# Performance work log

Measured on AMD Instinct MI355X. Metric: run time of the kernel, lower is better.

Reference implementation:

```python
import jax, jax.numpy as jnp
import numpy as np

B, T, D, H = 8, 1024, 1024, 16
HD = D // H
SCALE = HD ** -0.5


def setup_inputs() -> dict:
    key = jax.random.key(0)
    ks = jax.random.split(key, 5)
    s = 0.02
    return {
        "hidden_states": jax.random.normal(ks[0], (B, T, D), jnp.float32),
        "Wq": jax.random.normal(ks[1], (D, D), jnp.float32) * s,
        "bq": jnp.zeros((D,), jnp.float32),
        "Wk": jax.random.normal(ks[2], (D, D), jnp.float32) * s,
        "bk": jnp.zeros((D,), jnp.float32),
        "Wv": jax.random.normal(ks[3], (D, D), jnp.float32) * s,
        "bv": jnp.zeros((D,), jnp.float32),
        "Wo": jax.random.normal(ks[4], (D, D), jnp.float32) * s,
        "bo": jnp.zeros((D,), jnp.float32),
    }


def _split_heads(x):
    # [B, T, D] -> [B, H, T, HD]
    return x.reshape(B, T, H, HD).transpose(0, 2, 1, 3)


def reference(hidden_states, Wq, bq, Wk, bk, Wv, bv, Wo, bo):
    q = _split_heads((hidden_states @ Wq + bq) * SCALE)
    k = _split_heads(hidden_states @ Wk + bk)
    v = _split_heads(hidden_states @ Wv + bv)
    # [B, H, T, T] attention scores
    scores = jnp.einsum("bhqd,bhkd->bhqk", q, k)
    probs = jax.nn.softmax(scores, axis=-1)
    attn = jnp.einsum("bhqk,bhkd->bhqd", probs, v)
    attn = attn.transpose(0, 2, 1, 3).reshape(B, T, D)
    return attn @ Wo + bo
```

## Files before the change

kernel.cpp:

```cpp
#include <hip/hip_runtime.h>

typedef unsigned short u16;
typedef __attribute__((ext_vector_type(4))) float f32x4;
typedef __attribute__((ext_vector_type(8))) __bf16 bf16x8;
typedef __attribute__((ext_vector_type(4))) __bf16 bf16x4;
typedef __attribute__((ext_vector_type(4))) unsigned short u16x4;
typedef __attribute__((ext_vector_type(8))) unsigned short u16x8;

static __device__ __forceinline__ u16 f2bf(float f) {
    union { float f; unsigned u; } v; v.f = f;
    unsigned r = v.u + 0x7FFFu + ((v.u >> 16) & 1u);
    return (u16)(r >> 16);
}

static __device__ __forceinline__ float exp2f_fast(float x) {
    float r; asm("v_exp_f32 %0, %1" : "=v"(r) : "v"(x)); return r;
}

static __device__ __forceinline__ void gload16(const u16* g, u16* l) {
    __builtin_amdgcn_global_load_lds(
        (const __attribute__((address_space(1))) unsigned int*)g,
        (__attribute__((address_space(3))) unsigned int*)l, 16, 0, 0);
}

template<int N> static __device__ __forceinline__ void vm_wait() {
    if constexpr (N >= 8)      asm volatile("s_waitcnt vmcnt(8)" ::: "memory");
    else if constexpr (N == 6) asm volatile("s_waitcnt vmcnt(6)" ::: "memory");
    else if constexpr (N == 4) asm volatile("s_waitcnt vmcnt(4)" ::: "memory");
    else if constexpr (N == 3) asm volatile("s_waitcnt vmcnt(3)" ::: "memory");
    else if constexpr (N == 2) asm volatile("s_waitcnt vmcnt(2)" ::: "memory");
    else                       asm volatile("s_waitcnt vmcnt(0)" ::: "memory");
}

#define SWZ64(row, ec) (((row) * 64) + ((((ec) ^ ((row) & 7))) << 3))

__global__ __launch_bounds__(256) void k_prep(
    const float* __restrict__ hs, u16* __restrict__ Xb,
    const float* __restrict__ W0, const float* __restrict__ W1,
    const float* __restrict__ W2, const float* __restrict__ W3,
    u16* __restrict__ T0, u16* __restrict__ T1, u16* __restrict__ T2, u16* __restrict__ T3,
    float s0) {
    __shared__ float tile[32][33];
    const int id = blockIdx.x;
    const int tid = threadIdx.x;
    if (id < 8192) {
        size_t i = (size_t)id * 256 + tid;
        float4 v = ((const float4*)hs)[i];
        u16x4 o; o[0] = f2bf(v.x); o[1] = f2bf(v.y); o[2] = f2bf(v.z); o[3] = f2bf(v.w);
        *(u16x4*)(Xb + i * 4) = o;
        return;
    }
    const int wid = id - 8192;
    const int z = wid >> 10, rem = wid & 1023;
    const int n0 = (rem & 31) * 32, k0 = (rem >> 5) * 32;
    const float* W; u16* Tt; float sc;
    switch (z) {
        case 0:  W = W0; Tt = T0; sc = s0;  break;
        case 1:  W = W1; Tt = T1; sc = 1.f; break;
        case 2:  W = W2; Tt = T2; sc = 1.f; break;
        default: W = W3; Tt = T3; sc = 1.f; break;
    }
    int r = tid >> 3, c = (tid & 7) * 4;
    float4 v = *(const float4*)(W + (size_t)(k0 + r) * 1024 + n0 + c);
    tile[r][c] = v.x; tile[r][c + 1] = v.y; tile[r][c + 2] = v.z; tile[r][c + 3] = v.w;
    __syncthreads();
    u16x4 o;
    o[0] = f2bf(tile[c][r] * sc);
    o[1] = f2bf(tile[c + 1][r] * sc);
    o[2] = f2bf(tile[c + 2][r] * sc);
    o[3] = f2bf(tile[c + 3][r] * sc);
    *(u16x4*)(Tt + (size_t)(n0 + r) * 1024 + k0 + c) = o;
}

template<int BN>
__global__ __launch_bounds__(512, 2) void k_g256(
    const u16* __restrict__ A, const u16* __restrict__ Bt,
    const float* __restrict__ bias, const float* __restrict__ biasK, float qscale,
    u16* __restrict__ obf, u16* __restrict__ obK, float* __restrict__ of32,
    int ldc, int bias_row, int nblk, int mode) {
    constexpr int WN = (BN == 256) ? 4 : 2;
    constexpr int WAVE_M = (BN == 256) ? 128 : 64;
    constexpr int M_REP = WAVE_M / 16;
    constexpr int BCALLS = BN / 128;
    constexpr int LPT = 2 + BCALLS;
    constexpr int ASLOT = 256 * 32;
    constexpr int BSLOT = BN * 32;
    __shared__ u16 As[4 * ASLOT];
    __shared__ u16 Bs[4 * BSLOT];
    const int tid = threadIdx.x;
    const int l = tid & 63, w = tid >> 6;
    const int mw = w / WN, nw = w % WN;
    const int fr = l & 15, gg = l >> 4, f4 = gg * 4;
    const int id = blockIdx.x;
    const int swz = (id & 7) * 32 + (id >> 3);
    const int bm = swz / nblk, bn = swz % nblk;
    const size_t m0 = (size_t)bm * 256, n0v = (size_t)bn * BN;

    const int srow = w * 16 + (l >> 2);
    const int schk = ((l & 3) ^ ((l >> 3) & 3)) * 8;
    const u16* agp0 = A + (m0 + srow) * 1024 + schk;
    const u16* agp1 = A + (m0 + 128 + srow) * 1024 + schk;
    const u16* bgp0 = Bt + (n0v + srow) * 1024 + schk;
    const u16* bgp1 = (BN == 256) ? Bt + (n0v + 128 + srow) * 1024 + schk : bgp0;
    const int ldst = w * 512 + l * 8;

    const int fchk = (gg ^ ((fr >> 1) & 3)) * 8;
    int aoff[8], boff[4];
#pragma unroll
    for (int mt = 0; mt < 8; ++mt) aoff[mt] = (mw * WAVE_M + mt * 16 + fr) * 32 + fchk;
#pragma unroll
    for (int nt = 0; nt < 4; ++nt) boff[nt] = (nw * 64 + nt * 16 + fr) * 32 + fchk;

    f32x4 acc[8][4] = {};

#define PSTG(S, J)                                                              \
    gload16(agp0 + (size_t)(J) * 32, As + (S) * ASLOT + ldst);                  \
    gload16(agp1 + (size_t)(J) * 32, As + (S) * ASLOT + 4096 + ldst);           \
    gload16(bgp0 + (size_t)(J) * 32, Bs + (S) * BSLOT + ldst);                  \
    if constexpr (BN == 256)                                                    \
        gload16(bgp1 + (size_t)(J) * 32, Bs + (S) * BSLOT + 4096 + ldst);
    PSTG(0, 0) PSTG(1, 1) PSTG(2, 2)
#undef PSTG

#define TILE(S, J, VMN, STG)                                                    \
    {                                                                           \
        vm_wait<VMN>();                                                         \
        __builtin_amdgcn_s_barrier();                                           \
        bf16x8 afr[4], bfr[4];                                                  \
        _Pragma("unroll")                                                       \
        for (int nt = 0; nt < 4; ++nt)                                          \
            bfr[nt] = *(const bf16x8*)(&Bs[(S) * BSLOT + boff[nt]]);            \
        _Pragma("unroll")                                                       \
        for (int mt = 0; mt < 4; ++mt)                                          \
            afr[mt] = *(const bf16x8*)(&As[(S) * ASLOT + aoff[mt]]);            \
        if constexpr (STG) {                                                    \
            gload16(agp0 + (size_t)((J) + 3) * 32, As + (((S) + 3) & 3) * ASLOT + ldst);        \
            gload16(agp1 + (size_t)((J) + 3) * 32, As + (((S) + 3) & 3) * ASLOT + 4096 + ldst); \
            if constexpr (BN == 128)                                            \
                gload16(bgp0 + (size_t)((J) + 3) * 32, Bs + (((S) + 3) & 3) * BSLOT + ldst);    \
        }                                                                       \
        __builtin_amdgcn_s_barrier();                                           \
        asm volatile("s_waitcnt lgkmcnt(0)" ::: "memory");                      \
        __builtin_amdgcn_sched_barrier(0);                                      \
        __builtin_amdgcn_s_setprio(1);                                          \
        _Pragma("unroll")                                                       \
        for (int mt = 0; mt < 4; ++mt)                                          \
            _Pragma("unroll")                                                   \
            for (int nt = 0; nt < 4; ++nt)                                      \
                acc[mt][nt] = __builtin_amdgcn_mfma_f32_16x16x32_bf16(afr[mt], bfr[nt], acc[mt][nt], 0, 0, 0); \
        __builtin_amdgcn_s_setprio(0);                                          \
        if constexpr (BN == 256) {                                              \
            _Pragma("unroll")                                                   \
            for (int mt = 0; mt < 4; ++mt)                                      \
                afr[mt] = *(const bf16x8*)(&As[(S) * ASLOT + aoff[4 + mt]]);    \
            if constexpr (STG) {                                                \
                gload16(bgp0 + (size_t)((J) + 3) * 32, Bs + (((S) + 3) & 3) * BSLOT + ldst);        \
                gload16(bgp1 + (size_t)((J) + 3) * 32, Bs + (((S) + 3) & 3) * BSLOT + 4096 + ldst); \
            }                                                                   \
            __builtin_amdgcn_s_barrier();                                       \
            asm volatile("s_waitcnt lgkmcnt(0)" ::: "memory");                  \
            __builtin_amdgcn_sched_barrier(0);                                  \
            __builtin_amdgcn_s_setprio(1);                                      \
            _Pragma("unroll")                                                   \
            for (int mt = 0; mt < 4; ++mt)                                      \
                _Pragma("unroll")                                               \
                for (int nt = 0; nt < 4; ++nt)                                  \
                    acc[4 + mt][nt] = __builtin_amdgcn_mfma_f32_16x16x32_bf16(afr[mt], bfr[nt], acc[4 + mt][nt], 0, 0, 0); \
            __builtin_amdgcn_s_setprio(0);                                      \
        }                                                                       \
    }

#pragma unroll 1
    for (int jb = 0; jb < 28; jb += 4) {
        TILE(0, jb + 0, (2 * LPT), true)
        TILE(1, jb + 1, (2 * LPT), true)
        TILE(2, jb + 2, (2 * LPT), true)
        TILE(3, jb + 3, (2 * LPT), true)
    }
    TILE(0, 28, (2 * LPT), true)
    TILE(1, 29, (2 * LPT), false)
    TILE(2, 30, LPT, false)
    TILE(3, 31, 0, false)
#undef TILE

    const int mrow0 = (int)m0 + mw * WAVE_M;
    const int ncol0 = (int)n0v + nw * 64;
    if (mode == 1) {
#pragma unroll
        for (int mt = 0; mt < M_REP; ++mt)
#pragma unroll
            for (int nt = 0; nt < 4; ++nt) {
                const int col = ncol0 + nt * 16 + fr;
                const int seg = col >> 10, colm = col & 1023;
                const float bb = (seg ? biasK[colm] : bias[colm] * qscale);
                u16* op = seg ? obK : obf;
#pragma unroll
                for (int r = 0; r < 4; ++r)
                    op[(size_t)(mrow0 + mt * 16 + f4 + r) * 1024 + colm] = f2bf(acc[mt][nt][r] + bb);
            }
    } else if (mode == 2) {
#pragma unroll
        for (int mt = 0; mt < M_REP; ++mt) {
            float rb_[4];
#pragma unroll
            for (int r = 0; r < 4; ++r) rb_[r] = bias[mrow0 + mt * 16 + f4 + r];
#pragma unroll
            for (int nt = 0; nt < 4; ++nt) {
                const int col = ncol0 + nt * 16 + fr;
                const int colp = (col & ~31) | (((col >> 2) & 3) << 3) |
                                 (((col >> 4) & 1) << 2) | (col & 3);
#pragma unroll
                for (int r = 0; r < 4; ++r) {
                    const size_t row = (size_t)(mrow0 + mt * 16 + f4 + r);
                    obf[row * (size_t)ldc + colp] = f2bf(acc[mt][nt][r] + rb_[r]);
                }
            }
        }
    } else {
#pragma unroll
        for (int mt = 0; mt < M_REP; ++mt) {
            float rb_[4];
#pragma unroll
            for (int r = 0; r < 4; ++r)
                rb_[r] = bias_row ? bias[mrow0 + mt * 16 + f4 + r] : 0.f;
#pragma unroll
            for (int nt = 0; nt < 4; ++nt) {
                const int col = ncol0 + nt * 16 + fr;
                const float cb = bias_row ? 0.f : bias[col];
#pragma unroll
                for (int r = 0; r < 4; ++r) {
                    const size_t row = (size_t)(mrow0 + mt * 16 + f4 + r);
                    const float vv = acc[mt][nt][r] + cb + rb_[r];
                    if (of32) of32[row * (size_t)ldc + col] = vv;
                    else      obf[row * (size_t)ldc + col] = f2bf(vv);
                }
            }
        }
    }
}

static __device__ __forceinline__ void qk_tile(const u16* Ks, int fr, int gg,
                                               bf16x8 qA0, bf16x8 qA1, bf16x8 qB0, bf16x8 qB1,
                                               float mA, float mB, f32x4 sA[4], f32x4 sB[4]) {
    __builtin_amdgcn_s_setprio(1);
#pragma unroll
    for (int nt = 0; nt < 4; ++nt) {
        const int rk = nt * 16 + fr;
        const bf16x8 kf0 = *(const bf16x8*)(&Ks[SWZ64(rk, gg)]);
        const bf16x8 kf1 = *(const bf16x8*)(&Ks[SWZ64(rk, gg + 4)]);
        f32x4 z = {-mA, -mA, -mA, -mA};
        z = __builtin_amdgcn_mfma_f32_16x16x32_bf16(kf0, qA0, z, 0, 0, 0);
        z = __builtin_amdgcn_mfma_f32_16x16x32_bf16(kf1, qA1, z, 0, 0, 0);
        sA[nt] = z;
        f32x4 y = {-mB, -mB, -mB, -mB};
        y = __builtin_amdgcn_mfma_f32_16x16x32_bf16(kf0, qB0, y, 0, 0, 0);
        y = __builtin_amdgcn_mfma_f32_16x16x32_bf16(kf1, qB1, y, 0, 0, 0);
        sB[nt] = y;
    }
    __builtin_amdgcn_s_setprio(0);
}

static __device__ __forceinline__ void sm_tile(const f32x4 s[4], f32x4 o[4],
                                               float& m, float& lsum, bf16x4 p[4]) {
    float mymax = s[0][0];
#pragma unroll
    for (int nt = 0; nt < 4; ++nt)
#pragma unroll
        for (int r = 0; r < 4; ++r) mymax = fmaxf(mymax, s[nt][r]);
    float ps = 0.f;
#pragma unroll
    for (int nt = 0; nt < 4; ++nt)
#pragma unroll
        for (int r = 0; r < 4; ++r) {
            const float pp = exp2f_fast(s[nt][r]);
            ps += pp; p[nt][r] = (__bf16)pp;
        }
    if (__builtin_expect(__any(mymax > 11.0f), 0)) {
        float rm = fmaxf(mymax, __shfl_xor(mymax, 16, 64));
        rm = fmaxf(rm, __shfl_xor(rm, 32, 64));
        const float d = fmaxf(rm, 0.f);
        const float fac = exp2f_fast(-d);
        m += d; lsum *= fac;
#pragma unroll
        for (int mt = 0; mt < 4; ++mt)
#pragma unroll
            for (int r = 0; r < 4; ++r) o[mt][r] *= fac;
        ps = 0.f;
#pragma unroll
        for (int nt = 0; nt < 4; ++nt)
#pragma unroll
            for (int r = 0; r < 4; ++r) {
                const float pp = exp2f_fast(s[nt][r] - d);
                ps += pp; p[nt][r] = (__bf16)pp;
            }
    }
    lsum += ps;
}

static __device__ __forceinline__ void pv_tile(const u16* Vs, int fr, int gg,
                                               const bf16x4 pA[4], const bf16x4 pB[4],
                                               f32x4 oA[4], f32x4 oB[4]) {
    const bf16x8 BA0 = __builtin_shufflevector(pA[0], pA[1], 0, 1, 2, 3, 4, 5, 6, 7);
    const bf16x8 BA1 = __builtin_shufflevector(pA[2], pA[3], 0, 1, 2, 3, 4, 5, 6, 7);
    const bf16x8 BB0 = __builtin_shufflevector(pB[0], pB[1], 0, 1, 2, 3, 4, 5, 6, 7);
    const bf16x8 BB1 = __builtin_shufflevector(pB[2], pB[3], 0, 1, 2, 3, 4, 5, 6, 7);
    __builtin_amdgcn_s_setprio(1);
#pragma unroll
    for (int mt = 0; mt < 4; ++mt) {
        const int rv = mt * 16 + fr;
        const bf16x8 vk0 = *(const bf16x8*)(&Vs[SWZ64(rv, gg)]);
        const bf16x8 vk1 = *(const bf16x8*)(&Vs[SWZ64(rv, gg + 4)]);
        oA[mt] = __builtin_amdgcn_mfma_f32_16x16x32_bf16(vk0, BA0, oA[mt], 0, 0, 0);
        oA[mt] = __builtin_amdgcn_mfma_f32_16x16x32_bf16(vk1, BA1, oA[mt], 0, 0, 0);
        oB[mt] = __builtin_amdgcn_mfma_f32_16x16x32_bf16(vk0, BB0, oB[mt], 0, 0, 0);
        oB[mt] = __builtin_amdgcn_mfma_f32_16x16x32_bf16(vk1, BB1, oB[mt], 0, 0, 0);
    }
    __builtin_amdgcn_s_setprio(0);
}

__global__ __launch_bounds__(256, 2) void k_flash(const u16* __restrict__ Q, const u16* __restrict__ K,
                                                  const u16* __restrict__ Vt2, u16* __restrict__ O) {
    __shared__ u16 Ks[2][64 * 64];
    __shared__ u16 Vs[3][64 * 64];
    const int tid = threadIdx.x;
    const int l = tid & 63, w = tid >> 6;
    const int id = blockIdx.x;
    const int swz = (id & 7) * 128 + (id >> 3);
    const int bh = swz >> 3, qt = swz & 7;
    const int b = bh >> 4, h = bh & 15;
    const int qw = qt * 128 + w * 32;
    const int fr = l & 15, gg = l >> 4, f4 = gg * 4, f8 = gg * 8;

    const u16* qpA = Q + ((size_t)(b * 1024 + qw + fr)) * 1024 + h * 64 + f8;
    const u16* qpB = qpA + 16 * 1024;
    const bf16x8 qA0 = *(const bf16x8*)qpA;
    const bf16x8 qA1 = *(const bf16x8*)(qpA + 32);
    const bf16x8 qB0 = *(const bf16x8*)qpB;
    const bf16x8 qB1 = *(const bf16x8*)(qpB + 32);

    const int jj0 = w * 2, jj1 = w * 2 + 1;
    const int sr0 = jj0 * 8 + (l >> 3), sr1 = jj1 * 8 + (l >> 3);
    const int sc = ((l & 7) ^ (l >> 3)) * 8;
    const u16* kg0 = K + ((size_t)(b * 1024 + sr0)) * 1024 + h * 64 + sc;
    const u16* kg1 = K + ((size_t)(b * 1024 + sr1)) * 1024 + h * 64 + sc;
    const u16* vg0 = Vt2 + ((size_t)(h * 64 + sr0)) * 8192 + b * 1024 + sc;
    const u16* vg1 = Vt2 + ((size_t)(h * 64 + sr1)) * 8192 + b * 1024 + sc;
    const int lk0 = jj0 * 512 + l * 8, lk1 = jj1 * 512 + l * 8;

#define FSTGK(S, kt)                                        \
    gload16(kg0 + (size_t)(kt) * 1024, Ks[S] + lk0);        \
    gload16(kg1 + (size_t)(kt) * 1024, Ks[S] + lk1);
#define FSTGV(S, kt)                                        \
    gload16(vg0 + (kt), Vs[S] + lk0);                       \
    gload16(vg1 + (kt), Vs[S] + lk1);

    f32x4 oA[4] = {}, oB[4] = {};
    float mA = 0.f, lA = 0.f, mB = 0.f, lB = 0.f;
    bf16x4 p0A[4], p0B[4], p1A[4], p1B[4];

    FSTGK(0, 0) FSTGV(0, 0)

#define FITER(T, QS, PS, KS, VS, PCA, PCB, PPA, PPB, DOPV, DOSTG)            \
    {                                                                        \
        vm_wait<2>();                                                        \
        __builtin_amdgcn_s_barrier();                                        \
        f32x4 sA[4], sB[4];                                                  \
        qk_tile(Ks[QS], fr, gg, qA0, qA1, qB0, qB1, mA, mB, sA, sB);         \
        if (DOSTG) { FSTGK(KS, ((T) + 1) * 64) FSTGV(VS, ((T) + 1) * 64) }   \
        if (DOPV) pv_tile(Vs[PS], fr, gg, PPA, PPB, oA, oB);                 \
        sm_tile(sA, oA, mA, lA, PCA);                                        \
        sm_tile(sB, oB, mB, lB, PCB);                                        \
    }

    FITER(0,  0, 0, 1, 1, p0A, p0B, p1A, p1B, 0, 1)
    FITER(1,  1, 0, 0, 2, p1A, p1B, p0A, p0B, 1, 1)
    FITER(2,  0, 1, 1, 0, p0A, p0B, p1A, p1B, 1, 1)
    FITER(3,  1, 2, 0, 1, p1A, p1B, p0A, p0B, 1, 1)
    FITER(4,  0, 0, 1, 2, p0A, p0B, p1A, p1B, 1, 1)
    FITER(5,  1, 1, 0, 0, p1A, p1B, p0A, p0B, 1, 1)
    FITER(6,  0, 2, 1, 1, p0A, p0B, p1A, p1B, 1, 1)
    FITER(7,  1, 0, 0, 2, p1A, p1B, p0A, p0B, 1, 1)
    FITER(8,  0, 1, 1, 0, p0A, p0B, p1A, p1B, 1, 1)
    FITER(9,  1, 2, 0, 1, p1A, p1B, p0A, p0B, 1, 1)
    FITER(10, 0, 0, 1, 2, p0A, p0B, p1A, p1B, 1, 1)
    FITER(11, 1, 1, 0, 0, p1A, p1B, p0A, p0B, 1, 1)
    FITER(12, 0, 2, 1, 1, p0A, p0B, p1A, p1B, 1, 1)
    FITER(13, 1, 0, 0, 2, p1A, p1B, p0A, p0B, 1, 1)
    FITER(14, 0, 1, 1, 0, p0A, p0B, p1A, p1B, 1, 1)
    FITER(15, 1, 2, 0, 0, p1A, p1B, p0A, p0B, 1, 0)
#undef FITER
    vm_wait<0>();
    __builtin_amdgcn_s_barrier();
    pv_tile(Vs[0], fr, gg, p1A, p1B, oA, oB);
#undef FSTGK
#undef FSTGV

    lA += __shfl_xor(lA, 16, 64); lA += __shfl_xor(lA, 32, 64);
    lB += __shfl_xor(lB, 16, 64); lB += __shfl_xor(lB, 32, 64);
    const float ivA = 1.0f / lA, ivB = 1.0f / lB;
    u16* opA = O + ((size_t)(b * 1024 + qw + fr)) * 1024 + h * 64;
    u16* opB = opA + 16 * 1024;
#pragma unroll
    for (int mt = 0; mt < 4; ++mt) {
        u16x4 oa, ob;
#pragma unroll
        for (int r = 0; r < 4; ++r) { oa[r] = f2bf(oA[mt][r] * ivA); ob[r] = f2bf(oB[mt][r] * ivB); }
        *(u16x4*)(opA + mt * 16 + f4) = oa;
        *(u16x4*)(opB + mt * 16 + f4) = ob;
    }
}

extern "C" void kernel_launch(void* const* d_in, const int* in_sizes, int n_in,
                              void* d_out, int out_size, void* d_ws, size_t ws_size,
                              hipStream_t stream) {
    (void)in_sizes; (void)n_in; (void)out_size; (void)ws_size;
    const float* hs = (const float*)d_in[0];
    const float* Wq = (const float*)d_in[1];
    const float* bq = (const float*)d_in[2];
    const float* Wk = (const float*)d_in[3];
    const float* bk = (const float*)d_in[4];
    const float* Wv = (const float*)d_in[5];
    const float* bv = (const float*)d_in[6];
    const float* Wo = (const float*)d_in[7];
    const float* bo = (const float*)d_in[8];
    float* out = (float*)d_out;
    char* ws = (char*)d_ws;
    const size_t MB = 1024ull * 1024ull;
    u16* Xb  = (u16*)(ws);
    u16* Wqt = (u16*)(ws + 16 * MB);
    u16* Wkt = (u16*)(ws + 18 * MB);
    u16* Wvt = (u16*)(ws + 20 * MB);
    u16* Wot = (u16*)(ws + 22 * MB);
    u16* Qb  = (u16*)(ws + 24 * MB);
    u16* Kb  = (u16*)(ws + 40 * MB);
    u16* Vt2 = (u16*)(ws + 56 * MB);
    u16* Ob  = Xb;

    const float SCALE_Q = 0.125f * 1.4426950408889634f;

    k_prep<<<dim3(12288), dim3(256), 0, stream>>>(hs, Xb, Wq, Wk, Wv, Wo,
                                                  Wqt, Wkt, Wvt, Wot, SCALE_Q);
    k_g256<256><<<dim3(256), dim3(512), 0, stream>>>(Xb, Wqt, bq, bk, SCALE_Q,
                                                     Qb, Kb, nullptr, 1024, 0, 8, 1);
    k_g256<128><<<dim3(256), dim3(512), 0, stream>>>(Wvt, Xb, bv, nullptr, 1.f,
                                                     Vt2, nullptr, nullptr, 8192, 1, 64, 2);
    k_flash<<<dim3(1024), dim3(256), 0, stream>>>(Qb, Kb, Vt2, Ob);
    k_g256<128><<<dim3(256), dim3(512), 0, stream>>>(Ob, Wot, bo, nullptr, 1.f,
                                                     nullptr, nullptr, out, 1024, 0, 8, 0);
}
```

Before: 145.7 us.

## Replace 256x256 QK GEMM with 256x128 tiles, triple-buffered pipeline, higher occupancy

Drops the templated 256-wide GEMM variant and uses one 256x128 tile kernel for all projections. The QK projection now launches twice as many blocks, and the swizzle stride is passed in as a parameter. The shared-memory pipeline shrinks from four stages with prefetch distance 3 to three stages with distance 2. Launch bounds are raised to allow four blocks per CU in both the GEMM and flash kernels, and the softmax row-sum is split into four partial accumulators to shorten the dependency chain. Smaller tiles and a shallower pipeline raise occupancy, at the cost of less operand reuse and less latency hiding, and the tighter launch bounds could cause register spills.

```diff
diff --git a/kernel.cpp b/kernel.cpp
--- a/kernel.cpp
+++ b/kernel.cpp
@@ -24,10 +24,7 @@
 }
 
 template<int N> static __device__ __forceinline__ void vm_wait() {
-    if constexpr (N >= 8)      asm volatile("s_waitcnt vmcnt(8)" ::: "memory");
-    else if constexpr (N == 6) asm volatile("s_waitcnt vmcnt(6)" ::: "memory");
-    else if constexpr (N == 4) asm volatile("s_waitcnt vmcnt(4)" ::: "memory");
-    else if constexpr (N == 3) asm volatile("s_waitcnt vmcnt(3)" ::: "memory");
+    if constexpr (N == 3)      asm volatile("s_waitcnt vmcnt(3)" ::: "memory");
     else if constexpr (N == 2) asm volatile("s_waitcnt vmcnt(2)" ::: "memory");
     else                       asm volatile("s_waitcnt vmcnt(0)" ::: "memory");
 }
@@ -72,57 +69,47 @@
     *(u16x4*)(Tt + (size_t)(n0 + r) * 1024 + k0 + c) = o;
 }
 
-template<int BN>
-__global__ __launch_bounds__(512, 2) void k_g256(
+__global__ __launch_bounds__(512, 4) void k_g128(
     const u16* __restrict__ A, const u16* __restrict__ Bt,
     const float* __restrict__ bias, const float* __restrict__ biasK, float qscale,
     u16* __restrict__ obf, u16* __restrict__ obK, float* __restrict__ of32,
-    int ldc, int bias_row, int nblk, int mode) {
-    constexpr int WN = (BN == 256) ? 4 : 2;
-    constexpr int WAVE_M = (BN == 256) ? 128 : 64;
-    constexpr int M_REP = WAVE_M / 16;
-    constexpr int BCALLS = BN / 128;
-    constexpr int LPT = 2 + BCALLS;
+    int ldc, int bias_row, int nblk, int cpx, int mode) {
     constexpr int ASLOT = 256 * 32;
-    constexpr int BSLOT = BN * 32;
-    __shared__ u16 As[4 * ASLOT];
-    __shared__ u16 Bs[4 * BSLOT];
+    constexpr int BSLOT = 128 * 32;
+    __shared__ u16 As[3 * ASLOT];
+    __shared__ u16 Bs[3 * BSLOT];
     const int tid = threadIdx.x;
     const int l = tid & 63, w = tid >> 6;
-    const int mw = w / WN, nw = w % WN;
+    const int mw = w >> 1, nw = w & 1;
     const int fr = l & 15, gg = l >> 4, f4 = gg * 4;
     const int id = blockIdx.x;
-    const int swz = (id & 7) * 32 + (id >> 3);
+    const int swz = (id & 7) * cpx + (id >> 3);
     const int bm = swz / nblk, bn = swz % nblk;
-    const size_t m0 = (size_t)bm * 256, n0v = (size_t)bn * BN;
+    const size_t m0 = (size_t)bm * 256, n0v = (size_t)bn * 128;
 
     const int srow = w * 16 + (l >> 2);
     const int schk = ((l & 3) ^ ((l >> 3) & 3)) * 8;
     const u16* agp0 = A + (m0 + srow) * 1024 + schk;
     const u16* agp1 = A + (m0 + 128 + srow) * 1024 + schk;
     const u16* bgp0 = Bt + (n0v + srow) * 1024 + schk;
-    const u16* bgp1 = (BN == 256) ? Bt + (n0v + 128 + srow) * 1024 + schk : bgp0;
     const int ldst = w * 512 + l * 8;
 
     const int fchk = (gg ^ ((fr >> 1) & 3)) * 8;
-    int aoff[8], boff[4];
-#pragma unroll
-    for (int mt = 0; mt < 8; ++mt) aoff[mt] = (mw * WAVE_M + mt * 16 + fr) * 32 + fchk;
+    int aoff[4], boff[4];
+#pragma unroll
+    for (int mt = 0; mt < 4; ++mt) aoff[mt] = (mw * 64 + mt * 16 + fr) * 32 + fchk;
 #pragma unroll
     for (int nt = 0; nt < 4; ++nt) boff[nt] = (nw * 64 + nt * 16 + fr) * 32 + fchk;
 
-    f32x4 acc[8][4] = {};
-
-#define PSTG(S, J)                                                              \
+    f32x4 acc[4][4] = {};
+
+#define GSTG(S, J)                                                              \
     gload16(agp0 + (size_t)(J) * 32, As + (S) * ASLOT + ldst);                  \
     gload16(agp1 + (size_t)(J) * 32, As + (S) * ASLOT + 4096 + ldst);           \
-    gload16(bgp0 + (size_t)(J) * 32, Bs + (S) * BSLOT + ldst);                  \
-    if constexpr (BN == 256)                                                    \
-        gload16(bgp1 + (size_t)(J) * 32, Bs + (S) * BSLOT + 4096 + ldst);
-    PSTG(0, 0) PSTG(1, 1) PSTG(2, 2)
-#undef PSTG
-
-#define TILE(S, J, VMN, STG)                                                    \
+    gload16(bgp0 + (size_t)(J) * 32, Bs + (S) * BSLOT + ldst);
+    GSTG(0, 0) GSTG(1, 1)
+
+#define TILE(S, SD, J, VMN, STG)                                                \
     {                                                                           \
         vm_wait<VMN>();                                                         \
         __builtin_amdgcn_s_barrier();                                           \
@@ -133,12 +120,7 @@
         _Pragma("unroll")                                                       \
         for (int mt = 0; mt < 4; ++mt)                                          \
             afr[mt] = *(const bf16x8*)(&As[(S) * ASLOT + aoff[mt]]);            \
-        if constexpr (STG) {                                                    \
-            gload16(agp0 + (size_t)((J) + 3) * 32, As + (((S) + 3) & 3) * ASLOT + ldst);        \
-            gload16(agp1 + (size_t)((J) + 3) * 32, As + (((S) + 3) & 3) * ASLOT + 4096 + ldst); \
-            if constexpr (BN == 128)                                            \
-                gload16(bgp0 + (size_t)((J) + 3) * 32, Bs + (((S) + 3) & 3) * BSLOT + ldst);    \
-        }                                                                       \
+        if (STG) { GSTG(SD, (J) + 2) }                                          \
         __builtin_amdgcn_s_barrier();                                           \
         asm volatile("s_waitcnt lgkmcnt(0)" ::: "memory");                      \
         __builtin_amdgcn_sched_barrier(0);                                      \
@@ -149,45 +131,24 @@
             for (int nt = 0; nt < 4; ++nt)                                      \
                 acc[mt][nt] = __builtin_amdgcn_mfma_f32_16x16x32_bf16(afr[mt], bfr[nt], acc[mt][nt], 0, 0, 0); \
         __builtin_amdgcn_s_setprio(0);                                          \
-        if constexpr (BN == 256) {                                              \
-            _Pragma("unroll")                                                   \
-            for (int mt = 0; mt < 4; ++mt)                                      \
-                afr[mt] = *(const bf16x8*)(&As[(S) * ASLOT + aoff[4 + mt]]);    \
-            if constexpr (STG) {                                                \
-                gload16(bgp0 + (size_t)((J) + 3) * 32, Bs + (((S) + 3) & 3) * BSLOT + ldst);        \
-                gload16(bgp1 + (size_t)((J) + 3) * 32, Bs + (((S) + 3) & 3) * BSLOT + 4096 + ldst); \
-            }                                                                   \
-            __builtin_amdgcn_s_barrier();                                       \
-            asm volatile("s_waitcnt lgkmcnt(0)" ::: "memory");                  \
-            __builtin_amdgcn_sched_barrier(0);                                  \
-            __builtin_amdgcn_s_setprio(1);                                      \
-            _Pragma("unroll")                                                   \
-            for (int mt = 0; mt < 4; ++mt)                                      \
-                _Pragma("unroll")                                               \
-                for (int nt = 0; nt < 4; ++nt)                                  \
-                    acc[4 + mt][nt] = __builtin_amdgcn_mfma_f32_16x16x32_bf16(afr[mt], bfr[nt], acc[4 + mt][nt], 0, 0, 0); \
-            __builtin_amdgcn_s_setprio(0);                                      \
-        }                                                                       \
     }
 
 #pragma unroll 1
-    for (int jb = 0; jb < 28; jb += 4) {
-        TILE(0, jb + 0, (2 * LPT), true)
-        TILE(1, jb + 1, (2 * LPT), true)
-        TILE(2, jb + 2, (2 * LPT), true)
-        TILE(3, jb + 3, (2 * LPT), true)
-    }
-    TILE(0, 28, (2 * LPT), true)
-    TILE(1, 29, (2 * LPT), false)
-    TILE(2, 30, LPT, false)
-    TILE(3, 31, 0, false)
+    for (int jb = 0; jb < 30; jb += 3) {
+        TILE(0, 2, jb + 0, 3, true)
+        TILE(1, 0, jb + 1, 3, true)
+        TILE(2, 1, jb + 2, 3, true)
+    }
+    TILE(0, 2, 30, 3, false)
+    TILE(1, 0, 31, 0, false)
 #undef TILE
-
-    const int mrow0 = (int)m0 + mw * WAVE_M;
+#undef GSTG
+
+    const int mrow0 = (int)m0 + mw * 64;
     const int ncol0 = (int)n0v + nw * 64;
     if (mode == 1) {
 #pragma unroll
-        for (int mt = 0; mt < M_REP; ++mt)
+        for (int mt = 0; mt < 4; ++mt)
 #pragma unroll
             for (int nt = 0; nt < 4; ++nt) {
                 const int col = ncol0 + nt * 16 + fr;
@@ -200,7 +161,7 @@
             }
     } else if (mode == 2) {
 #pragma unroll
-        for (int mt = 0; mt < M_REP; ++mt) {
+        for (int mt = 0; mt < 4; ++mt) {
             float rb_[4];
 #pragma unroll
             for (int r = 0; r < 4; ++r) rb_[r] = bias[mrow0 + mt * 16 + f4 + r];
@@ -218,7 +179,7 @@
         }
     } else {
 #pragma unroll
-        for (int mt = 0; mt < M_REP; ++mt) {
+        for (int mt = 0; mt < 4; ++mt) {
             float rb_[4];
 #pragma unroll
             for (int r = 0; r < 4; ++r)
@@ -267,14 +228,15 @@
     for (int nt = 0; nt < 4; ++nt)
 #pragma unroll
         for (int r = 0; r < 4; ++r) mymax = fmaxf(mymax, s[nt][r]);
-    float ps = 0.f;
+    float psn[4] = {0.f, 0.f, 0.f, 0.f};
 #pragma unroll
     for (int nt = 0; nt < 4; ++nt)
 #pragma unroll
         for (int r = 0; r < 4; ++r) {
             const float pp = exp2f_fast(s[nt][r]);
-            ps += pp; p[nt][r] = (__bf16)pp;
+            psn[nt] += pp; p[nt][r] = (__bf16)pp;
         }
+    float ps = (psn[0] + psn[1]) + (psn[2] + psn[3]);
     if (__builtin_expect(__any(mymax > 11.0f), 0)) {
         float rm = fmaxf(mymax, __shfl_xor(mymax, 16, 64));
         rm = fmaxf(rm, __shfl_xor(rm, 32, 64));
@@ -318,7 +280,7 @@
     __builtin_amdgcn_s_setprio(0);
 }
 
-__global__ __launch_bounds__(256, 2) void k_flash(const u16* __restrict__ Q, const u16* __restrict__ K,
+__global__ __launch_bounds__(256, 4) void k_flash(const u16* __restrict__ Q, const u16* __restrict__ K,
                                                   const u16* __restrict__ Vt2, u16* __restrict__ O) {
     __shared__ u16 Ks[2][64 * 64];
     __shared__ u16 Vs[3][64 * 64];
@@ -440,11 +402,11 @@
 
     k_prep<<<dim3(12288), dim3(256), 0, stream>>>(hs, Xb, Wq, Wk, Wv, Wo,
                                                   Wqt, Wkt, Wvt, Wot, SCALE_Q);
-    k_g256<256><<<dim3(256), dim3(512), 0, stream>>>(Xb, Wqt, bq, bk, SCALE_Q,
-                                                     Qb, Kb, nullptr, 1024, 0, 8, 1);
-    k_g256<128><<<dim3(256), dim3(512), 0, stream>>>(Wvt, Xb, bv, nullptr, 1.f,
-                                                     Vt2, nullptr, nullptr, 8192, 1, 64, 2);
+    k_g128<<<dim3(512), dim3(512), 0, stream>>>(Xb, Wqt, bq, bk, SCALE_Q,
+                                                Qb, Kb, nullptr, 1024, 0, 16, 64, 1);
+    k_g128<<<dim3(256), dim3(512), 0, stream>>>(Wvt, Xb, bv, nullptr, 1.f,
+                                                Vt2, nullptr, nullptr, 8192, 1, 64, 32, 2);
     k_flash<<<dim3(1024), dim3(256), 0, stream>>>(Qb, Kb, Vt2, Ob);
-    k_g256<128><<<dim3(256), dim3(512), 0, stream>>>(Ob, Wot, bo, nullptr, 1.f,
-                                                     nullptr, nullptr, out, 1024, 0, 8, 0);
-}
+    k_g128<<<dim3(256), dim3(512), 0, stream>>>(Ob, Wot, bo, nullptr, 1.f,
+                                                nullptr, nullptr, out, 1024, 0, 8, 32, 0);
+}
```

Result: slower. 156.8 us (+7.6%).
